# Optimization experiments

Measured on AMD Instinct MI355X. Metric: run time of the kernel, lower is better.

## Reference

```python
import jax, jax.numpy as jnp
import numpy as np

H = 128           # hidden_size
N_NODE = 100000   # item vocab
B = 1024          # sessions
NODES_PER = 50
N = B * NODES_PER # total session nodes
E = 8 * N         # edges


def setup_inputs() -> dict:
    key = jax.random.key(0)
    ks = jax.random.split(key, 16)
    stdv = 1.0 / np.sqrt(H)
    u = lambda k, shape: jax.random.uniform(k, shape, jnp.float32, -stdv, stdv)
    x = jax.random.randint(ks[0], (N,), 1, N_NODE + 1)      # 1-indexed items
    edge_index = jax.random.randint(ks[1], (2, E), 0, N)
    batch = jnp.repeat(jnp.arange(B), NODES_PER)            # sorted segment ids
    return {
        "x": x, "edge_index": edge_index, "batch": batch,
        "emb_weight": u(ks[2], (N_NODE, H)),
        "W_gconv": u(ks[3], (H, H)),
        "W_ih": u(ks[4], (3 * H, H)), "W_hh": u(ks[5], (3 * H, H)),
        "b_ih": u(ks[6], (3 * H,)), "b_hh": u(ks[7], (3 * H,)),
        "W1_w": u(ks[8], (H, H)), "W1_b": u(ks[9], (H,)),
        "W2_w": u(ks[10], (H, H)), "W2_b": u(ks[11], (H,)),
        "q_w": u(ks[12], (1, H)), "q_b": u(ks[13], (1,)),
        "W3_w": u(ks[14], (H, 2 * H)), "W3_b": u(ks[15], (H,)),
    }


def _forward(x, edge_index, batch, emb_weight, W_gconv, W_ih, W_hh, b_ih, b_hh,
             W1_w, W1_b, W2_w, W2_b, q_w, q_b, W3_w, W3_b):
    n = x.shape[0]
    h = emb_weight[x - 1]                                   # [N, H]
    # GatedGraphConv, num_layers=1: linear -> scatter-add -> GRUCell
    m = h @ W_gconv                                          # [N, H]
    agg = jax.ops.segment_sum(m[edge_index[0]], edge_index[1], num_segments=n)
    gi = agg @ W_ih.T + b_ih                                 # [N, 3H]
    gh = h @ W_hh.T + b_hh
    i_r, i_z, i_n = jnp.split(gi, 3, axis=1)
    h_r, h_z, h_n = jnp.split(gh, 3, axis=1)
    r = jax.nn.sigmoid(i_r + h_r)
    z = jax.nn.sigmoid(i_z + h_z)
    ng = jnp.tanh(i_n + r * h_n)
    h = (1.0 - z) * ng + z * h
    h = jax.nn.relu(h)
    # Embedding2Score: segment-wise attention readout
    last_idx = jax.ops.segment_max(jnp.arange(n), batch, num_segments=B)
    v_n = h[last_idx]                                        # [B, H] last node per session
    a = jax.nn.sigmoid(v_n[batch] @ W1_w.T + W1_b + h @ W2_w.T + W2_b)
    alpha = a @ q_w.T + q_b                                  # [N, 1]
    s_g = jax.ops.segment_sum(alpha * h, batch, num_segments=B)  # [B, H]
    s_h = jnp.concatenate([v_n, s_g], axis=1) @ W3_w.T + W3_b    # [B, H]
    return s_h @ emb_weight.T                                # [B, n_node]


def reference(x, edge_index, batch, emb_weight, W_gconv, W_ih, W_hh, b_ih, b_hh,
              W1_w, W1_b, W2_w, W2_b, q_w, q_b, W3_w, W3_b):
    return _forward(x, edge_index, batch, emb_weight, W_gconv, W_ih, W_hh, b_ih, b_hh,
                    W1_w, W1_b, W2_w, W2_b, q_w, q_b, W3_w, W3_b)
```

## Files before the change

### kernel.cpp

```cpp
#include <hip/hip_runtime.h>
#include <math.h>

#define NNODES 51200
#define NEDGES 409600
#define NB 1024
#define NODES_PER 50
#define NVOCAB 100000
#define NVPAD 100096
#define SLOTS 64

typedef __attribute__((ext_vector_type(8))) short bf16x8;
typedef __attribute__((ext_vector_type(4))) float f32x4;

__device__ __forceinline__ float sigf(float x) { return 1.0f / (1.0f + __expf(-x)); }

__device__ __forceinline__ ushort f2bf(float x) {
    union { float f; unsigned u; } v; v.f = x;
    const unsigned r = v.u + 0x7FFF + ((v.u >> 16) & 1);
    return (ushort)(r >> 16);
}
__device__ __forceinline__ float bf2f(ushort u) {
    union { float f; unsigned u; } v; v.u = ((unsigned)u) << 16; return v.f;
}
__device__ __forceinline__ bf16x8 cvt8(const float* __restrict__ src) {
    const float4 v0 = *(const float4*)src, v1 = *(const float4*)(src + 4);
    bf16x8 p;
    p[0] = (short)f2bf(v0.x); p[1] = (short)f2bf(v0.y);
    p[2] = (short)f2bf(v0.z); p[3] = (short)f2bf(v0.w);
    p[4] = (short)f2bf(v1.x); p[5] = (short)f2bf(v1.y);
    p[6] = (short)f2bf(v1.z); p[7] = (short)f2bf(v1.w);
    return p;
}

__global__ __launch_bounds__(256)
void prep_kernel(const int* __restrict__ x, const float* __restrict__ emb,
                 ushort* __restrict__ hb, const int* __restrict__ ei,
                 int* __restrict__ cnt, int* __restrict__ esrc,
                 ushort* __restrict__ embswz, const float* __restrict__ Wih,
                 const float* __restrict__ Wg, ushort* __restrict__ Wc) {
    const int bid = blockIdx.x;
    const int t = threadIdx.x;
    if (bid < 3200) {
        const int tid = bid * 256 + t;
        const int i = tid >> 4, c8 = (tid & 15) * 8;
        const int idx = x[i] - 1;
        *(bf16x8*)(hb + (size_t)i * 128 + c8) = cvt8(emb + (size_t)idx * 128 + c8);
    } else if (bid < 4800) {
        const int e = (bid - 3200) * 256 + t;
        const int dst = ei[NEDGES + e];
        const int pos = atomicAdd(&cnt[dst], 1);
        if (pos < SLOTS) esrc[(size_t)dst * SLOTS + pos] = ei[e];
    } else if (bid < 11056) {
        const int f = (bid - 4800) * 256 + t;
        const int row = f >> 4, c8 = (f & 15) * 8;
        bf16x8 pk = {0, 0, 0, 0, 0, 0, 0, 0};
        if (row < NVOCAB) pk = cvt8(emb + (size_t)row * 128 + c8);
        *(bf16x8*)&embswz[(size_t)row * 128 + (c8 ^ ((row & 7) << 3))] = pk;
    } else {
        const int idx = (bid - 11056) * 256 + t;
        const int mrow = idx >> 7, n = idx & 127;
        const float* wr = Wih + (size_t)mrow * 128;
        const float* gr = Wg + (size_t)n * 128;
        float acc = 0.f;
        #pragma unroll 8
        for (int k = 0; k < 128; ++k)
            acc = fmaf(wr[k], gr[k], acc);
        Wc[idx] = f2bf(acc);
    }
}

__global__ __launch_bounds__(256)
void agg_kernel(const int* __restrict__ cnt, const int* __restrict__ esrc,
                const ushort* __restrict__ hb, ushort* __restrict__ aggb) {
    const int node = blockIdx.x * 4 + (threadIdx.x >> 6);
    const int l = threadIdx.x & 63;
    int cn = cnt[node]; if (cn > SLOTS) cn = SLOTS;
    const int* es = esrc + (size_t)node * SLOTS;
    float ax = 0.f, ay = 0.f;
    for (int j = 0; j < cn; ++j) {
        const int src = es[j];
        const unsigned u = *(const unsigned*)(hb + (size_t)src * 128 + l * 2);
        ax += bf2f((ushort)(u & 0xffff));
        ay += bf2f((ushort)(u >> 16));
    }
    const unsigned o = (unsigned)f2bf(ax) | ((unsigned)f2bf(ay) << 16);
    *(unsigned*)(aggb + (size_t)node * 128 + l * 2) = o;
}

__global__ __launch_bounds__(512)
void gru_fused(const ushort* __restrict__ aggb, const ushort* __restrict__ Wc,
               const float* __restrict__ Whh, const float* __restrict__ bih,
               const float* __restrict__ bhh, ushort* __restrict__ hb) {
    __shared__ ushort As[128 * 128];
    __shared__ ushort Bs[384 * 128];
    const int m0 = blockIdx.x * 128;
    const int t = threadIdx.x;
    const int lane = t & 63, wid = t >> 6;
    const int l15 = lane & 15, kg = (lane >> 4) * 8;

    #pragma unroll
    for (int f = t; f < 2048; f += 512) {
        const int r = f >> 4, c8 = (f & 15) * 8;
        const bf16x8 pk = *(const bf16x8*)(aggb + (size_t)(m0 + r) * 128 + c8);
        *(bf16x8*)&As[r * 128 + (c8 ^ ((r & 7) << 3))] = pk;
    }
    #pragma unroll
    for (int f = t; f < 6144; f += 512) {
        const int r = f >> 4, c8 = (f & 15) * 8;
        const bf16x8 pk = *(const bf16x8*)(Wc + (size_t)r * 128 + c8);
        *(bf16x8*)&Bs[r * 128 + (c8 ^ ((r & 7) << 3))] = pk;
    }
    __syncthreads();

    f32x4 gi[24] = {};
    #pragma unroll
    for (int kc = 0; kc < 4; ++kc) {
        const int cs = kc * 32 + kg;
        const int ra = wid * 16 + l15;
        const bf16x8 af = *(const bf16x8*)&As[ra * 128 + (cs ^ ((ra & 7) << 3))];
        #pragma unroll
        for (int j = 0; j < 24; ++j) {
            const int rb = j * 16 + l15;
            const bf16x8 bfr = *(const bf16x8*)&Bs[rb * 128 + (cs ^ ((rb & 7) << 3))];
            gi[j] = __builtin_amdgcn_mfma_f32_16x16x32_bf16(af, bfr, gi[j], 0, 0, 0);
        }
    }
    __syncthreads();

    #pragma unroll
    for (int f = t; f < 2048; f += 512) {
        const int r = f >> 4, c8 = (f & 15) * 8;
        const bf16x8 pk = *(const bf16x8*)(hb + (size_t)(m0 + r) * 128 + c8);
        *(bf16x8*)&As[r * 128 + (c8 ^ ((r & 7) << 3))] = pk;
    }
    #pragma unroll
    for (int f = t; f < 6144; f += 512) {
        const int r = f >> 4, c8 = (f & 15) * 8;
        *(bf16x8*)&Bs[r * 128 + (c8 ^ ((r & 7) << 3))] = cvt8(Whh + (size_t)r * 128 + c8);
    }
    __syncthreads();

    f32x4 gh[24] = {};
    #pragma unroll
    for (int kc = 0; kc < 4; ++kc) {
        const int cs = kc * 32 + kg;
        const int ra = wid * 16 + l15;
        const bf16x8 af = *(const bf16x8*)&As[ra * 128 + (cs ^ ((ra & 7) << 3))];
        #pragma unroll
        for (int j = 0; j < 24; ++j) {
            const int rb = j * 16 + l15;
            const bf16x8 bfr = *(const bf16x8*)&Bs[rb * 128 + (cs ^ ((rb & 7) << 3))];
            gh[j] = __builtin_amdgcn_mfma_f32_16x16x32_bf16(af, bfr, gh[j], 0, 0, 0);
        }
    }

    const int lr0 = wid * 16 + (lane >> 4) * 4;
    #pragma unroll
    for (int j = 0; j < 8; ++j) {
        const int col = j * 16 + l15;
        const float bir = bih[col], biz = bih[128 + col], bin = bih[256 + col];
        const float bhr = bhh[col], bhz = bhh[128 + col], bhn = bhh[256 + col];
        #pragma unroll
        for (int q = 0; q < 4; ++q) {
            const int lr = lr0 + q;
            const int adr = lr * 128 + (col ^ ((lr & 7) << 3));
            const float hv = bf2f(As[adr]);
            const float r_ = sigf(gi[j][q] + bir + gh[j][q] + bhr);
            const float z  = sigf(gi[j + 8][q] + biz + gh[j + 8][q] + bhz);
            const float ng = tanhf(gi[j + 16][q] + bin + r_ * (gh[j + 16][q] + bhn));
            As[adr] = f2bf(fmaxf((1.f - z) * ng + z * hv, 0.f));
        }
    }
    __syncthreads();
    #pragma unroll
    for (int f = t; f < 2048; f += 512) {
        const int r = f >> 4, c8 = (f & 15) * 8;
        *(bf16x8*)(hb + (size_t)(m0 + r) * 128 + c8) =
            *(const bf16x8*)&As[r * 128 + (c8 ^ ((r & 7) << 3))];
    }
}

__global__ __launch_bounds__(256)
void attn_sh(const ushort* __restrict__ hb, const float* __restrict__ W1,
             const float* __restrict__ b1, const float* __restrict__ W2,
             const float* __restrict__ qw, const float* __restrict__ qbp,
             const float* __restrict__ b2, const float* __restrict__ W3,
             const float* __restrict__ b3, ushort* __restrict__ shb) {
    __shared__ ushort As[128 * 128];
    __shared__ ushort Bs[128 * 128];
    __shared__ float t1s[2][128];
    __shared__ float qws[128];
    __shared__ float apar[2][2][64];
    __shared__ float alph[2][64];
    __shared__ float sgs[2][128];
    const int m0 = blockIdx.x * 100;
    const int t = threadIdx.x;
    const int lane = t & 63, wid = t >> 6;
    const int wr = wid >> 1, wc = wid & 1;
    const int l15 = lane & 15, kg = (lane >> 4) * 8;
    const int cr0 = (lane >> 4) * 4;

    #pragma unroll
    for (int f = t; f < 2048; f += 256) {
        const int r = f >> 4, c8 = (f & 15) * 8;
        int gr = m0 + r; if (gr > NNODES - 1) gr = NNODES - 1;
        *(bf16x8*)&As[r * 128 + (c8 ^ ((r & 7) << 3))] =
            *(const bf16x8*)(hb + (size_t)gr * 128 + c8);
        *(bf16x8*)&Bs[r * 128 + (c8 ^ ((r & 7) << 3))] = cvt8(W2 + (size_t)r * 128 + c8);
    }
    if (t < 128) qws[t] = qw[t];
    __syncthreads();

    f32x4 acc[4][4] = {};
    #pragma unroll
    for (int kc = 0; kc < 4; ++kc) {
        const int cs = kc * 32 + kg;
        bf16x8 af[4], bfr[4];
        #pragma unroll
        for (int i = 0; i < 4; ++i) {
            const int ra = wr * 64 + i * 16 + l15;
            af[i] = *(const bf16x8*)&As[ra * 128 + (cs ^ ((ra & 7) << 3))];
            const int rb = wc * 64 + i * 16 + l15;
            bfr[i] = *(const bf16x8*)&Bs[rb * 128 + (cs ^ ((rb & 7) << 3))];
        }
        #pragma unroll
        for (int i = 0; i < 4; ++i)
            #pragma unroll
            for (int j = 0; j < 4; ++j)
                acc[i][j] = __builtin_amdgcn_mfma_f32_16x16x32_bf16(af[i], bfr[j], acc[i][j], 0, 0, 0);
    }
    __syncthreads();

    #pragma unroll
    for (int j = 0; j < 4; ++j) {
        const int col = wc * 64 + j * 16 + l15;
        const int csw = (col & 7) << 3;
        #pragma unroll
        for (int i = 0; i < 4; ++i) {
            const int row = wr * 64 + i * 16 + cr0;
            #pragma unroll
            for (int q = 0; q < 4; ++q)
                Bs[col * 128 + ((row + q) ^ csw)] = f2bf(acc[i][j][q]);
        }
    }

    const int sess = wid >> 1, half = wid & 1;
    const int d = half * 64 + lane;
    const int vrow = sess * 50 + 49;
    const int vsw = (vrow & 7) << 3;
    float t1v = b1[d] + b2[d];
    const float* w1r = W1 + (size_t)d * 128;
    #pragma unroll 8
    for (int k = 0; k < 128; k += 4) {
        const float4 w = *(const float4*)(w1r + k);
        t1v += w.x * bf2f(As[vrow * 128 + ((k + 0) ^ vsw)])
             + w.y * bf2f(As[vrow * 128 + ((k + 1) ^ vsw)])
             + w.z * bf2f(As[vrow * 128 + ((k + 2) ^ vsw)])
             + w.w * bf2f(As[vrow * 128 + ((k + 3) ^ vsw)]);
    }
    t1s[sess][d] = t1v;
    __syncthreads();

    float p = 0.f;
    if (lane < 50) {
        const int row = sess * 50 + lane;
        const int d0 = half * 64;
        #pragma unroll 8
        for (int dd = d0; dd < d0 + 64; ++dd)
            p += qws[dd] * sigf(t1s[sess][dd] + bf2f(Bs[dd * 128 + (row ^ ((dd & 7) << 3))]));
    }
    apar[sess][half][lane] = p;
    __syncthreads();
    if (half == 0 && lane < 50)
        alph[sess][lane] = apar[sess][0][lane] + apar[sess][1][lane] + qbp[0];
    __syncthreads();

    float sacc = 0.f;
    #pragma unroll 10
    for (int i = 0; i < 50; ++i) {
        const int row = sess * 50 + i;
        sacc += alph[sess][i] * bf2f(As[row * 128 + (d ^ ((row & 7) << 3))]);
    }
    sgs[sess][d] = sacc;
    __syncthreads();

    float shacc = b3[d];
    const float* w3r = W3 + (size_t)d * 256;
    #pragma unroll 8
    for (int k = 0; k < 128; k += 4) {
        const float4 w = *(const float4*)(w3r + k);
        shacc += w.x * bf2f(As[vrow * 128 + ((k + 0) ^ vsw)])
               + w.y * bf2f(As[vrow * 128 + ((k + 1) ^ vsw)])
               + w.z * bf2f(As[vrow * 128 + ((k + 2) ^ vsw)])
               + w.w * bf2f(As[vrow * 128 + ((k + 3) ^ vsw)]);
    }
    #pragma unroll 8
    for (int k = 0; k < 128; k += 4) {
        const float4 w = *(const float4*)(w3r + 128 + k);
        shacc += w.x * sgs[sess][k] + w.y * sgs[sess][k + 1]
               + w.z * sgs[sess][k + 2] + w.w * sgs[sess][k + 3];
    }
    const int orow = blockIdx.x * 2 + sess;
    shb[(size_t)orow * 128 + (d ^ ((orow & 7) << 3))] = f2bf(shacc);
}

__global__ __launch_bounds__(512)
void gemm_vocab(float* __restrict__ C, const ushort* __restrict__ Ab,
                const ushort* __restrict__ Bswz) {
    __shared__ ushort As[128 * 128];
    __shared__ ushort Bs[128 * 128];
    __shared__ float Cs[128 * 132];
    const int id = blockIdx.x;
    const int xcd = id & 7, loc = id >> 3;
    const int mt = loc & 7, gin = loc >> 3;
    const int grp = xcd * 25 + gin;
    const int m0 = mt * 128;
    const int start = grp * 4;
    int nt = 782 - start; if (nt > 4) nt = 4;
    if (nt <= 0) return;
    const int t = threadIdx.x;
    const int lane = t & 63, wid = t >> 6;
    const int wm = wid >> 2, wn = wid & 3;
    const int l15 = lane & 15, kg = (lane >> 4) * 8;
    const int cr0 = (lane >> 4) * 4;

    #pragma unroll
    for (int f = t; f < 2048; f += 512)
        *(bf16x8*)&As[f * 8] = *(const bf16x8*)(Ab + (size_t)m0 * 128 + f * 8);
    {
        const ushort* srcb = Bswz + (size_t)start * 128 * 128;
        #pragma unroll
        for (int f = t; f < 2048; f += 512)
            *(bf16x8*)&Bs[f * 8] = *(const bf16x8*)(srcb + f * 8);
    }
    __syncthreads();

    for (int it = 0; it < nt; ++it) {
        const int n0 = (start + it) * 128;
        f32x4 acc[4][2] = {};
        #pragma unroll
        for (int kc = 0; kc < 4; ++kc) {
            const int cs = kc * 32 + kg;
            bf16x8 af[4], bfr[2];
            #pragma unroll
            for (int i = 0; i < 4; ++i) {
                const int ra = wm * 64 + i * 16 + l15;
                af[i] = *(const bf16x8*)&As[ra * 128 + (cs ^ ((ra & 7) << 3))];
            }
            #pragma unroll
            for (int j = 0; j < 2; ++j) {
                const int rb = wn * 32 + j * 16 + l15;
                bfr[j] = *(const bf16x8*)&Bs[rb * 128 + (cs ^ ((rb & 7) << 3))];
            }
            #pragma unroll
            for (int i = 0; i < 4; ++i)
                #pragma unroll
                for (int j = 0; j < 2; ++j)
                    acc[i][j] = __builtin_amdgcn_mfma_f32_16x16x32_bf16(af[i], bfr[j], acc[i][j], 0, 0, 0);
        }
        __syncthreads();

        #pragma unroll
        for (int j = 0; j < 2; ++j) {
            const int col = wn * 32 + j * 16 + l15;
            #pragma unroll
            for (int i = 0; i < 4; ++i) {
                const int row = wm * 64 + i * 16 + cr0;
                #pragma unroll
                for (int q = 0; q < 4; ++q)
                    Cs[(row + q) * 132 + col] = acc[i][j][q];
            }
        }
        if (it + 1 < nt) {
            const ushort* srcb = Bswz + (size_t)(n0 + 128) * 128;
            #pragma unroll
            for (int f = t; f < 2048; f += 512)
                *(bf16x8*)&Bs[f * 8] = *(const bf16x8*)(srcb + f * 8);
        }
        __syncthreads();

        #pragma unroll
        for (int f = t; f < 4096; f += 512) {
            const int r = f >> 5, c4 = (f & 31) * 4;
            if (n0 + c4 < NVOCAB) {
                const f32x4 v = *(const f32x4*)&Cs[r * 132 + c4];
                *(f32x4*)(C + (size_t)(m0 + r) * NVOCAB + n0 + c4) = v;
            }
        }
    }
}

extern "C" void kernel_launch(void* const* d_in, const int* in_sizes, int n_in,
                              void* d_out, int out_size, void* d_ws, size_t ws_size,
                              hipStream_t stream) {
    const int*   x   = (const int*)d_in[0];
    const int*   ei  = (const int*)d_in[1];
    const float* emb = (const float*)d_in[3];
    const float* Wg  = (const float*)d_in[4];
    const float* Wih = (const float*)d_in[5];
    const float* Whh = (const float*)d_in[6];
    const float* bih = (const float*)d_in[7];
    const float* bhh = (const float*)d_in[8];
    const float* W1  = (const float*)d_in[9];
    const float* b1  = (const float*)d_in[10];
    const float* W2  = (const float*)d_in[11];
    const float* b2  = (const float*)d_in[12];
    const float* qw  = (const float*)d_in[13];
    const float* qb  = (const float*)d_in[14];
    const float* W3  = (const float*)d_in[15];
    const float* b3  = (const float*)d_in[16];
    float* out = (float*)d_out;

    float*  ws     = (float*)d_ws;
    ushort* hb     = (ushort*)ws;
    ushort* aggb   = (ushort*)(ws + 3276800);
    ushort* Wc     = (ushort*)(ws + 6553600);
    ushort* shb    = (ushort*)(ws + 6578176);
    ushort* embswz = (ushort*)(ws + 6643712);
    int*    cnt    = (int*)(ws + 13049856);
    int*    esrc   = cnt + NNODES;

    hipMemsetAsync(cnt, 0, NNODES * sizeof(int), stream);

    prep_kernel<<<11248, 256, 0, stream>>>(x, emb, hb, ei, cnt, esrc, embswz,
                                           Wih, Wg, Wc);

    agg_kernel<<<12800, 256, 0, stream>>>(cnt, esrc, hb, aggb);

    gru_fused<<<400, 512, 0, stream>>>(aggb, Wc, Whh, bih, bhh, hb);

    attn_sh<<<512, 256, 0, stream>>>(hb, W1, b1, W2, qw, qb, b2, W3, b3, shb);

    gemm_vocab<<<1600, 512, 0, stream>>>(out, shb, embswz);
}
```

Before: 323.0 us.

## Shrink vocab GEMM to 256 threads and alias C staging onto B tile

The vocab GEMM drops from 512 to 256 threads, and each wave now computes a 64x64 tile instead of 64x32. The separate padded C staging buffer is removed and its data is staged through the B tile's shared memory in two 64-row halves. This cuts LDS use per block from about 130KB to 64KB so more blocks can be resident per CU. The cost is lost B prefetch overlap, extra barriers, an unpadded staging stride that can cause bank conflicts, and higher register pressure per thread.

Result: no change. 322.0 us (-0.3%).

```diff
diff --git a/kernel.cpp b/kernel.cpp
--- a/kernel.cpp
+++ b/kernel.cpp
@@ -304,88 +304,82 @@
     shb[(size_t)orow * 128 + (d ^ ((orow & 7) << 3))] = f2bf(shacc);
 }
 
-__global__ __launch_bounds__(512)
+__global__ __launch_bounds__(256)
 void gemm_vocab(float* __restrict__ C, const ushort* __restrict__ Ab,
                 const ushort* __restrict__ Bswz) {
     __shared__ ushort As[128 * 128];
     __shared__ ushort Bs[128 * 128];
-    __shared__ float Cs[128 * 132];
+    float* Cs = (float*)Bs;
     const int id = blockIdx.x;
     const int xcd = id & 7, loc = id >> 3;
     const int mt = loc & 7, gin = loc >> 3;
     const int grp = xcd * 25 + gin;
     const int m0 = mt * 128;
-    const int start = grp * 4;
-    int nt = 782 - start; if (nt > 4) nt = 4;
-    if (nt <= 0) return;
     const int t = threadIdx.x;
     const int lane = t & 63, wid = t >> 6;
-    const int wm = wid >> 2, wn = wid & 3;
+    const int wr = wid >> 1, wc = wid & 1;
     const int l15 = lane & 15, kg = (lane >> 4) * 8;
     const int cr0 = (lane >> 4) * 4;
 
     #pragma unroll
-    for (int f = t; f < 2048; f += 512)
+    for (int f = t; f < 2048; f += 256)
         *(bf16x8*)&As[f * 8] = *(const bf16x8*)(Ab + (size_t)m0 * 128 + f * 8);
-    {
-        const ushort* srcb = Bswz + (size_t)start * 128 * 128;
-        #pragma unroll
-        for (int f = t; f < 2048; f += 512)
+
+    for (int it = 0; it < 4; ++it) {
+        const int n0 = (grp * 4 + it) * 128;
+        if (n0 >= NVOCAB) break;
+        __syncthreads();
+        const ushort* srcb = Bswz + (size_t)n0 * 128;
+        #pragma unroll
+        for (int f = t; f < 2048; f += 256)
             *(bf16x8*)&Bs[f * 8] = *(const bf16x8*)(srcb + f * 8);
-    }
-    __syncthreads();
-
-    for (int it = 0; it < nt; ++it) {
-        const int n0 = (start + it) * 128;
-        f32x4 acc[4][2] = {};
+        __syncthreads();
+
+        f32x4 acc[4][4] = {};
         #pragma unroll
         for (int kc = 0; kc < 4; ++kc) {
             const int cs = kc * 32 + kg;
-            bf16x8 af[4], bfr[2];
+            bf16x8 af[4], bfr[4];
             #pragma unroll
             for (int i = 0; i < 4; ++i) {
-                const int ra = wm * 64 + i * 16 + l15;
+                const int ra = wr * 64 + i * 16 + l15;
                 af[i] = *(const bf16x8*)&As[ra * 128 + (cs ^ ((ra & 7) << 3))];
-            }
-            #pragma unroll
-            for (int j = 0; j < 2; ++j) {
-                const int rb = wn * 32 + j * 16 + l15;
-                bfr[j] = *(const bf16x8*)&Bs[rb * 128 + (cs ^ ((rb & 7) << 3))];
+                const int rb = wc * 64 + i * 16 + l15;
+                bfr[i] = *(const bf16x8*)&Bs[rb * 128 + (cs ^ ((rb & 7) << 3))];
             }
             #pragma unroll
             for (int i = 0; i < 4; ++i)
                 #pragma unroll
-                for (int j = 0; j < 2; ++j)
+                for (int j = 0; j < 4; ++j)
                     acc[i][j] = __builtin_amdgcn_mfma_f32_16x16x32_bf16(af[i], bfr[j], acc[i][j], 0, 0, 0);
         }
         __syncthreads();
 
         #pragma unroll
-        for (int j = 0; j < 2; ++j) {
-            const int col = wn * 32 + j * 16 + l15;
+        for (int half = 0; half < 2; ++half) {
+            if (wr == half) {
+                #pragma unroll
+                for (int j = 0; j < 4; ++j) {
+                    const int col = wc * 64 + j * 16 + l15;
+                    #pragma unroll
+                    for (int i = 0; i < 4; ++i) {
+                        const int rl = i * 16 + cr0;
+                        #pragma unroll
+                        for (int q = 0; q < 4; ++q)
+                            Cs[(rl + q) * 128 + col] = acc[i][j][q];
+                    }
+                }
+            }
+            __syncthreads();
             #pragma unroll
-            for (int i = 0; i < 4; ++i) {
-                const int row = wm * 64 + i * 16 + cr0;
-                #pragma unroll
-                for (int q = 0; q < 4; ++q)
-                    Cs[(row + q) * 132 + col] = acc[i][j][q];
+            for (int f = t; f < 2048; f += 256) {
+                const int r = f >> 5, c4 = (f & 31) * 4;
+                if (n0 + c4 < NVOCAB) {
+                    const f32x4 v = *(const f32x4*)&Cs[r * 128 + c4];
+                    *(f32x4*)(C + (size_t)(m0 + half * 64 + r) * NVOCAB + n0 + c4) = v;
+                }
             }
-        }
-        if (it + 1 < nt) {
-            const ushort* srcb = Bswz + (size_t)(n0 + 128) * 128;
-            #pragma unroll
-            for (int f = t; f < 2048; f += 512)
-                *(bf16x8*)&Bs[f * 8] = *(const bf16x8*)(srcb + f * 8);
-        }
-        __syncthreads();
-
-        #pragma unroll
-        for (int f = t; f < 4096; f += 512) {
-            const int r = f >> 5, c4 = (f & 31) * 4;
-            if (n0 + c4 < NVOCAB) {
-                const f32x4 v = *(const f32x4*)&Cs[r * 132 + c4];
-                *(f32x4*)(C + (size_t)(m0 + r) * NVOCAB + n0 + c4) = v;
-            }
+            __syncthreads();
         }
     }
 }
@@ -431,5 +425,5 @@
 
     attn_sh<<<512, 256, 0, stream>>>(hb, W1, b1, W2, qw, qb, b2, W3, b3, shb);
 
-    gemm_vocab<<<1600, 512, 0, stream>>>(out, shb, embswz);
-}
+    gemm_vocab<<<1600, 256, 0, stream>>>(out, shb, embswz);
+}
```
